# Optimization experiments

Hardware: AMD Instinct MI355X
Metric: run time of the kernel (lower is better)

## Reference

```python
import jax, jax.numpy as jnp
import numpy as np

# ProbAttention (Yangskm/DroneMA-i-), eval mode (dropout=identity).
# Key facts from the source: mask_flag=False, scale=None -> `if self.scale` is
# False, so scores are NOT divided by sqrt(D). The _prob_QK sampling/topk result
# `u` and _get_initial_context are dead code w.r.t. the returned context, so the
# output is exactly dense softmax attention. Inputs are (B, L, H, D); the module
# transposes to (B, H, L, D) and transposes back at the end.

def setup_inputs() -> dict:
    key = jax.random.key(0)
    k1, k2, k3 = jax.random.split(key, 3)
    B, L, H, D = 4, 2048, 8, 64
    return {
        "queries": jax.random.normal(k1, (B, L, H, D), dtype=jnp.float32),
        "keys": jax.random.normal(k2, (B, L, H, D), dtype=jnp.float32),
        "values": jax.random.normal(k3, (B, L, H, D), dtype=jnp.float32),
    }

def reference(queries, keys, values):
    # (B, L, H, D) -> (B, H, L, D)
    q = jnp.swapaxes(queries, 1, 2)
    k = jnp.swapaxes(keys, 1, 2)
    v = jnp.swapaxes(values, 1, 2)
    # dense scores, NO 1/sqrt(D) scaling (scale=None in the original)
    scores = jnp.einsum("bhqd,bhkd->bhqk", q, k)
    attn = jax.nn.softmax(scores, axis=-1)
    ctx = jnp.einsum("bhqk,bhkd->bhqd", attn, v)
    # back to (B, L, H, D)
    return jnp.swapaxes(ctx, 1, 2)
```

## Files before the change

kernel.cpp:

```cpp
#include <hip/hip_runtime.h>
#include <hip/hip_bf16.h>


#define B_ 4
#define L_ 2048
#define H_ 8
#define D_ 64
#define RST_ 512
#define QW_ 32
#define QB_ 128
#define KT_ 64
#define NT_ (L_ / KT_)
#define RS_ 88
#define OTS_ 68
#define SCW_ 35
#define LOG2E_ 1.44269504088896f

#define SMEM_BYTES 45056

typedef _Float16 f16x8 __attribute__((ext_vector_type(8)));
typedef short    s16x4 __attribute__((ext_vector_type(4)));
typedef short    s16x8 __attribute__((ext_vector_type(8)));
typedef float    f32x4 __attribute__((ext_vector_type(4)));

__device__ __forceinline__ unsigned pk_bf16(float a, float b) {
    const __bf16 x = (__bf16)a, y = (__bf16)b;
    return ((unsigned)__builtin_bit_cast(unsigned short, y) << 16) |
           (unsigned)__builtin_bit_cast(unsigned short, x);
}

__device__ __forceinline__ f32x4 mfma16_bf16(s16x4 a, s16x4 b, f32x4 c) {
    return __builtin_amdgcn_mfma_f32_16x16x16bf16_1k(a, b, c, 0, 0, 0);
}

__global__ __launch_bounds__(512, 4) void attn_dbuf_fix(
    const float* __restrict__ Qg, const float* __restrict__ Kg,
    const float* __restrict__ Vg, float* __restrict__ Og)
{
    __shared__ __align__(16) char smem[SMEM_BYTES];
    _Float16* Kf0 = (_Float16*)smem;
    _Float16* Kf1 = (_Float16*)(smem + 11264);
    __bf16*   Vt0 = (__bf16*)(smem + 22528);
    __bf16*   Vt1 = (__bf16*)(smem + 33792);
    float*    Sc  = (float*)smem;

    const int tid  = threadIdx.x;
    const int w    = tid >> 6;
    const int qsub = w & 3;
    const int ks   = w >> 2;
    const int ln   = tid & 15;
    const int lg   = (tid >> 4) & 3;

    const int blk   = (blockIdx.x & 7) * 64 + (blockIdx.x >> 3);
    const int qtile = blk & (L_ / QB_ - 1);
    const int bh    = blk >> 4;
    const int h     = bh & (H_ - 1);
    const int b     = bh >> 3;

    const size_t bhbase = (size_t)b * (L_ * H_ * D_) + (size_t)h * D_;
    const int    qbase  = qtile * QB_ + qsub * QW_;

    f16x8 qf[2][2];
#pragma unroll
    for (int ms = 0; ms < 2; ++ms) {
#pragma unroll
        for (int dc = 0; dc < 2; ++dc) {
            const float* src = Qg + bhbase
                + (size_t)(qbase + ms * 16 + ln) * RST_ + dc * 32 + lg * 8;
            const float4 a = ((const float4*)src)[0];
            const float4 c = ((const float4*)src)[1];
            f16x8 f;
            f[0] = (_Float16)(a.x * LOG2E_); f[1] = (_Float16)(a.y * LOG2E_);
            f[2] = (_Float16)(a.z * LOG2E_); f[3] = (_Float16)(a.w * LOG2E_);
            f[4] = (_Float16)(c.x * LOG2E_); f[5] = (_Float16)(c.y * LOG2E_);
            f[6] = (_Float16)(c.z * LOG2E_); f[7] = (_Float16)(c.w * LOG2E_);
            qf[ms][dc] = f;
        }
    }

    f32x4 o[2][4];
    f32x4 lsum[2];
#pragma unroll
    for (int ms = 0; ms < 2; ++ms) {
        lsum[ms] = (f32x4){0.f, 0.f, 0.f, 0.f};
#pragma unroll
        for (int dg = 0; dg < 4; ++dg) o[ms][dg] = (f32x4){0.f, 0.f, 0.f, 0.f};
    }

    s16x4 ones4;
#pragma unroll
    for (int j = 0; j < 4; ++j) ones4[j] = (short)0x3F80;

    const int krow = tid >> 3;
    const int kd8  = (tid & 7) * 8;
    const int vkp  = (tid & 31) * 2;
    const int vdb  = (tid >> 5) * 4;
    const int vpos = (vkp & 32) + (((vkp & 15) >> 2) * 8)
                   + (((vkp >> 4) & 1) * 4) + (vkp & 3);

    const float* kp = Kg + bhbase + (size_t)krow * RST_ + kd8;
    const float* vp = Vg + bhbase + (size_t)vkp * RST_ + vdb;

    float4 sk0, sk1, sv0, sv1;

    auto issue = [&]() {
        sk0 = ((const float4*)kp)[0];
        sk1 = ((const float4*)kp)[1];
        sv0 = ((const float4*)vp)[0];
        sv1 = ((const float4*)(vp + RST_))[0];
        kp += (size_t)KT_ * RST_;
        vp += (size_t)KT_ * RST_;
    };
    auto writeKV = [&](_Float16* Kf, __bf16* Vt) {
        f16x8 kw;
        kw[0] = (_Float16)sk0.x; kw[1] = (_Float16)sk0.y;
        kw[2] = (_Float16)sk0.z; kw[3] = (_Float16)sk0.w;
        kw[4] = (_Float16)sk1.x; kw[5] = (_Float16)sk1.y;
        kw[6] = (_Float16)sk1.z; kw[7] = (_Float16)sk1.w;
        *(f16x8*)&Kf[krow * RS_ + kd8] = kw;
        *(unsigned*)&Vt[(vdb + 0) * RS_ + vpos] = pk_bf16(sv0.x, sv1.x);
        *(unsigned*)&Vt[(vdb + 1) * RS_ + vpos] = pk_bf16(sv0.y, sv1.y);
        *(unsigned*)&Vt[(vdb + 2) * RS_ + vpos] = pk_bf16(sv0.z, sv1.z);
        *(unsigned*)&Vt[(vdb + 3) * RS_ + vpos] = pk_bf16(sv0.w, sv1.w);
    };

    f16x8 kfr[2][2];
    s16x8 vfp[4];
    auto readFrags = [&](const _Float16* Kf, const __bf16* Vt) {
#pragma unroll
        for (int dc = 0; dc < 2; ++dc)
#pragma unroll
            for (int kg = 0; kg < 2; ++kg)
                kfr[dc][kg] = *(const f16x8*)
                    &Kf[(ks * 32 + kg * 16 + ln) * RS_ + dc * 32 + lg * 8];
#pragma unroll
        for (int dg = 0; dg < 4; ++dg)
            vfp[dg] = *(const s16x8*)&Vt[(dg * 16 + ln) * RS_ + ks * 32 + lg * 8];
    };

    auto computeT = [&]() {
#pragma unroll
        for (int ms = 0; ms < 2; ++ms) {
            f32x4 st[2];
#pragma unroll
            for (int kg = 0; kg < 2; ++kg) st[kg] = (f32x4){0.f, 0.f, 0.f, 0.f};
            __builtin_amdgcn_s_setprio(1);
#pragma unroll
            for (int dc = 0; dc < 2; ++dc)
#pragma unroll
                for (int kg = 0; kg < 2; ++kg)
                    st[kg] = __builtin_amdgcn_mfma_f32_16x16x32_f16(
                        kfr[dc][kg], qf[ms][dc], st[kg], 0, 0, 0);
            __builtin_amdgcn_s_setprio(0);

            s16x4 pf[2];
#pragma unroll
            for (int kg = 0; kg < 2; ++kg) {
                const float p0 = __builtin_amdgcn_exp2f(st[kg][0]);
                const float p1 = __builtin_amdgcn_exp2f(st[kg][1]);
                const float p2 = __builtin_amdgcn_exp2f(st[kg][2]);
                const float p3 = __builtin_amdgcn_exp2f(st[kg][3]);
                union { unsigned u[2]; s16x4 v; } pu;
                pu.u[0] = pk_bf16(p0, p1);
                pu.u[1] = pk_bf16(p2, p3);
                pf[kg] = pu.v;
            }

            __builtin_amdgcn_s_setprio(1);
#pragma unroll
            for (int kg = 0; kg < 2; ++kg) {
                lsum[ms] = mfma16_bf16(ones4, pf[kg], lsum[ms]);
#pragma unroll
                for (int dg = 0; dg < 4; ++dg) {
                    const s16x4 vh = (kg == 0)
                        ? __builtin_shufflevector(vfp[dg], vfp[dg], 0, 1, 2, 3)
                        : __builtin_shufflevector(vfp[dg], vfp[dg], 4, 5, 6, 7);
                    o[ms][dg] = mfma16_bf16(vh, pf[kg], o[ms][dg]);
                }
            }
            __builtin_amdgcn_s_setprio(0);
        }
    };

    issue();
    writeKV(Kf0, Vt0);
    issue();
    __syncthreads();

    for (int t = 0; t < NT_; t += 2) {
        readFrags(Kf0, Vt0);
        writeKV(Kf1, Vt1);
        if (t + 2 < NT_) issue();
        computeT();
        __syncthreads();
        readFrags(Kf1, Vt1);
        if (t + 2 < NT_) writeKV(Kf0, Vt0);
        if (t + 3 < NT_) issue();
        computeT();
        __syncthreads();
    }

    const int lane = tid & 63;
    if (w >= 4) {
        float* sc = &Sc[((w - 4) * 64 + lane) * SCW_];
#pragma unroll
        for (int ms = 0; ms < 2; ++ms)
#pragma unroll
            for (int dg = 0; dg < 4; ++dg)
#pragma unroll
                for (int r = 0; r < 4; ++r)
                    sc[ms * 16 + dg * 4 + r] = o[ms][dg][r];
        sc[32] = lsum[0][0];
        sc[33] = lsum[1][0];
    }
    __syncthreads();
    if (w < 4) {
        const float* sc = &Sc[(w * 64 + lane) * SCW_];
        float po[2][4][4];
#pragma unroll
        for (int ms = 0; ms < 2; ++ms)
#pragma unroll
            for (int dg = 0; dg < 4; ++dg)
#pragma unroll
                for (int r = 0; r < 4; ++r)
                    po[ms][dg][r] = o[ms][dg][r] + sc[ms * 16 + dg * 4 + r];
        const float linv[2] = {1.0f / (lsum[0][0] + sc[32]),
                               1.0f / (lsum[1][0] + sc[33])};

        float* Ot = (float*)(smem + w * 8960);
        const int qr = lane >> 2;
        const int ch = lane & 3;
#pragma unroll
        for (int ms = 0; ms < 2; ++ms) {
#pragma unroll
            for (int dg = 0; dg < 4; ++dg) {
#pragma unroll
                for (int i = 0; i < 2; ++i) {
                    float2 pr;
                    pr.x = po[ms][dg][2 * i]     * linv[ms];
                    pr.y = po[ms][dg][2 * i + 1] * linv[ms];
                    *(float2*)&Ot[ln * OTS_ + dg * 16 + lg * 4 + 2 * i] = pr;
                }
            }
#pragma unroll
            for (int p = 0; p < 4; ++p) {
                const float4 vo = *(const float4*)&Ot[qr * OTS_ + ch * 4 + p * 16];
                *(float4*)(Og + bhbase
                    + (size_t)(qbase + ms * 16 + qr) * RST_ + ch * 4 + p * 16) = vo;
            }
        }
    }
}

extern "C" void kernel_launch(void* const* d_in, const int* in_sizes, int n_in,
                              void* d_out, int out_size, void* d_ws, size_t ws_size,
                              hipStream_t stream) {
    const float* Q = (const float*)d_in[0];
    const float* K = (const float*)d_in[1];
    const float* V = (const float*)d_in[2];
    float* O = (float*)d_out;

    const int grid = B_ * H_ * (L_ / QB_);
    attn_dbuf_fix<<<grid, 512, 0, stream>>>(Q, K, V, O);
}
```

Before: 63.86 us.

## Double block to 1024 threads with 16 query rows per wave

Doubles the threads per block to 1024 and gives each wave 16 query rows instead of 32. This cuts per-wave registers so more waves can be resident, hiding the latency of the LDS reads and the exp computations. K and V tile loading is now split so half the threads load K and half load V, and the V transpose drops the permuted position layout. Fragments are read from LDS inside the compute step rather than ahead of the writes, and the final reduction across the two K-split halves is adapted to 8 query subgroups. In exchange, each K/V fragment read from LDS now serves only 16 query rows, so LDS read traffic per flop doubles.

```diff
diff --git a/kernel.cpp b/kernel.cpp
--- a/kernel.cpp
+++ b/kernel.cpp
@@ -7,20 +7,19 @@
 #define H_ 8
 #define D_ 64
 #define RST_ 512
-#define QW_ 32
+#define QW_ 16
 #define QB_ 128
 #define KT_ 64
 #define NT_ (L_ / KT_)
 #define RS_ 88
 #define OTS_ 68
-#define SCW_ 35
+#define SCW_ 18
 #define LOG2E_ 1.44269504088896f
 
 #define SMEM_BYTES 45056
 
 typedef _Float16 f16x8 __attribute__((ext_vector_type(8)));
 typedef short    s16x4 __attribute__((ext_vector_type(4)));
-typedef short    s16x8 __attribute__((ext_vector_type(8)));
 typedef float    f32x4 __attribute__((ext_vector_type(4)));
 
 __device__ __forceinline__ unsigned pk_bf16(float a, float b) {
@@ -33,7 +32,7 @@
     return __builtin_amdgcn_mfma_f32_16x16x16bf16_1k(a, b, c, 0, 0, 0);
 }
 
-__global__ __launch_bounds__(512, 4) void attn_dbuf_fix(
+__global__ __launch_bounds__(1024, 8) void attn_occ8(
     const float* __restrict__ Qg, const float* __restrict__ Kg,
     const float* __restrict__ Vg, float* __restrict__ Og)
 {
@@ -46,8 +45,8 @@
 
     const int tid  = threadIdx.x;
     const int w    = tid >> 6;
-    const int qsub = w & 3;
-    const int ks   = w >> 2;
+    const int qsub = w & 7;
+    const int ks   = w >> 3;
     const int ln   = tid & 15;
     const int lg   = (tid >> 4) & 3;
 
@@ -60,124 +59,99 @@
     const size_t bhbase = (size_t)b * (L_ * H_ * D_) + (size_t)h * D_;
     const int    qbase  = qtile * QB_ + qsub * QW_;
 
-    f16x8 qf[2][2];
-#pragma unroll
-    for (int ms = 0; ms < 2; ++ms) {
-#pragma unroll
-        for (int dc = 0; dc < 2; ++dc) {
-            const float* src = Qg + bhbase
-                + (size_t)(qbase + ms * 16 + ln) * RST_ + dc * 32 + lg * 8;
-            const float4 a = ((const float4*)src)[0];
-            const float4 c = ((const float4*)src)[1];
-            f16x8 f;
-            f[0] = (_Float16)(a.x * LOG2E_); f[1] = (_Float16)(a.y * LOG2E_);
-            f[2] = (_Float16)(a.z * LOG2E_); f[3] = (_Float16)(a.w * LOG2E_);
-            f[4] = (_Float16)(c.x * LOG2E_); f[5] = (_Float16)(c.y * LOG2E_);
-            f[6] = (_Float16)(c.z * LOG2E_); f[7] = (_Float16)(c.w * LOG2E_);
-            qf[ms][dc] = f;
-        }
-    }
-
-    f32x4 o[2][4];
-    f32x4 lsum[2];
-#pragma unroll
-    for (int ms = 0; ms < 2; ++ms) {
-        lsum[ms] = (f32x4){0.f, 0.f, 0.f, 0.f};
-#pragma unroll
-        for (int dg = 0; dg < 4; ++dg) o[ms][dg] = (f32x4){0.f, 0.f, 0.f, 0.f};
-    }
+    f16x8 qf[2];
+#pragma unroll
+    for (int dc = 0; dc < 2; ++dc) {
+        const float* src = Qg + bhbase
+            + (size_t)(qbase + ln) * RST_ + dc * 32 + lg * 8;
+        const float4 a = ((const float4*)src)[0];
+        const float4 c = ((const float4*)src)[1];
+        f16x8 f;
+        f[0] = (_Float16)(a.x * LOG2E_); f[1] = (_Float16)(a.y * LOG2E_);
+        f[2] = (_Float16)(a.z * LOG2E_); f[3] = (_Float16)(a.w * LOG2E_);
+        f[4] = (_Float16)(c.x * LOG2E_); f[5] = (_Float16)(c.y * LOG2E_);
+        f[6] = (_Float16)(c.z * LOG2E_); f[7] = (_Float16)(c.w * LOG2E_);
+        qf[dc] = f;
+    }
+
+    f32x4 o[4];
+    f32x4 lsum;
+    lsum = (f32x4){0.f, 0.f, 0.f, 0.f};
+#pragma unroll
+    for (int dg = 0; dg < 4; ++dg) o[dg] = (f32x4){0.f, 0.f, 0.f, 0.f};
 
     s16x4 ones4;
 #pragma unroll
     for (int j = 0; j < 4; ++j) ones4[j] = (short)0x3F80;
 
-    const int krow = tid >> 3;
-    const int kd8  = (tid & 7) * 8;
-    const int vkp  = (tid & 31) * 2;
-    const int vdb  = (tid >> 5) * 4;
-    const int vpos = (vkp & 32) + (((vkp & 15) >> 2) * 8)
-                   + (((vkp >> 4) & 1) * 4) + (vkp & 3);
-
-    const float* kp = Kg + bhbase + (size_t)krow * RST_ + kd8;
-    const float* vp = Vg + bhbase + (size_t)vkp * RST_ + vdb;
-
-    float4 sk0, sk1, sv0, sv1;
+    const bool isK = (tid < 512);
+    const int  kt_ = tid & 511;
+    const int  krow = kt_ >> 3;
+    const int  kd8  = (kt_ & 7) * 8;
+    const int  vkp  = (kt_ & 31) * 2;
+    const int  vdb  = (kt_ >> 5) * 4;
+
+    const float* gp = isK
+        ? (Kg + bhbase + (size_t)krow * RST_ + kd8)
+        : (Vg + bhbase + (size_t)vkp * RST_ + vdb);
+    const int soff = isK ? 4 : RST_;
+
+    float4 s0, s1;
 
     auto issue = [&]() {
-        sk0 = ((const float4*)kp)[0];
-        sk1 = ((const float4*)kp)[1];
-        sv0 = ((const float4*)vp)[0];
-        sv1 = ((const float4*)(vp + RST_))[0];
-        kp += (size_t)KT_ * RST_;
-        vp += (size_t)KT_ * RST_;
+        s0 = ((const float4*)gp)[0];
+        s1 = *(const float4*)(gp + soff);
+        gp += (size_t)KT_ * RST_;
     };
     auto writeKV = [&](_Float16* Kf, __bf16* Vt) {
-        f16x8 kw;
-        kw[0] = (_Float16)sk0.x; kw[1] = (_Float16)sk0.y;
-        kw[2] = (_Float16)sk0.z; kw[3] = (_Float16)sk0.w;
-        kw[4] = (_Float16)sk1.x; kw[5] = (_Float16)sk1.y;
-        kw[6] = (_Float16)sk1.z; kw[7] = (_Float16)sk1.w;
-        *(f16x8*)&Kf[krow * RS_ + kd8] = kw;
-        *(unsigned*)&Vt[(vdb + 0) * RS_ + vpos] = pk_bf16(sv0.x, sv1.x);
-        *(unsigned*)&Vt[(vdb + 1) * RS_ + vpos] = pk_bf16(sv0.y, sv1.y);
-        *(unsigned*)&Vt[(vdb + 2) * RS_ + vpos] = pk_bf16(sv0.z, sv1.z);
-        *(unsigned*)&Vt[(vdb + 3) * RS_ + vpos] = pk_bf16(sv0.w, sv1.w);
+        if (isK) {
+            f16x8 kw;
+            kw[0] = (_Float16)s0.x; kw[1] = (_Float16)s0.y;
+            kw[2] = (_Float16)s0.z; kw[3] = (_Float16)s0.w;
+            kw[4] = (_Float16)s1.x; kw[5] = (_Float16)s1.y;
+            kw[6] = (_Float16)s1.z; kw[7] = (_Float16)s1.w;
+            *(f16x8*)&Kf[krow * RS_ + kd8] = kw;
+        } else {
+            *(unsigned*)&Vt[(vdb + 0) * RS_ + vkp] = pk_bf16(s0.x, s1.x);
+            *(unsigned*)&Vt[(vdb + 1) * RS_ + vkp] = pk_bf16(s0.y, s1.y);
+            *(unsigned*)&Vt[(vdb + 2) * RS_ + vkp] = pk_bf16(s0.z, s1.z);
+            *(unsigned*)&Vt[(vdb + 3) * RS_ + vkp] = pk_bf16(s0.w, s1.w);
+        }
     };
 
-    f16x8 kfr[2][2];
-    s16x8 vfp[4];
-    auto readFrags = [&](const _Float16* Kf, const __bf16* Vt) {
-#pragma unroll
-        for (int dc = 0; dc < 2; ++dc)
-#pragma unroll
-            for (int kg = 0; kg < 2; ++kg)
-                kfr[dc][kg] = *(const f16x8*)
-                    &Kf[(ks * 32 + kg * 16 + ln) * RS_ + dc * 32 + lg * 8];
-#pragma unroll
-        for (int dg = 0; dg < 4; ++dg)
-            vfp[dg] = *(const s16x8*)&Vt[(dg * 16 + ln) * RS_ + ks * 32 + lg * 8];
-    };
-
-    auto computeT = [&]() {
-#pragma unroll
-        for (int ms = 0; ms < 2; ++ms) {
-            f32x4 st[2];
-#pragma unroll
-            for (int kg = 0; kg < 2; ++kg) st[kg] = (f32x4){0.f, 0.f, 0.f, 0.f};
+    auto computeT = [&](const _Float16* Kf, const __bf16* Vt) {
+#pragma unroll
+        for (int kg = 0; kg < 2; ++kg) {
+            const int krow0 = (ks * 32 + kg * 16 + ln) * RS_;
+            const f16x8 ka = *(const f16x8*)&Kf[krow0 + lg * 8];
+            const f16x8 kb = *(const f16x8*)&Kf[krow0 + 32 + lg * 8];
+            const int vcol = ks * 32 + kg * 16 + lg * 4;
+            const s16x4 v0 = *(const s16x4*)&Vt[(0 * 16 + ln) * RS_ + vcol];
+            const s16x4 v1 = *(const s16x4*)&Vt[(1 * 16 + ln) * RS_ + vcol];
+            const s16x4 v2 = *(const s16x4*)&Vt[(2 * 16 + ln) * RS_ + vcol];
+            const s16x4 v3 = *(const s16x4*)&Vt[(3 * 16 + ln) * RS_ + vcol];
+
+            f32x4 st = (f32x4){0.f, 0.f, 0.f, 0.f};
             __builtin_amdgcn_s_setprio(1);
-#pragma unroll
-            for (int dc = 0; dc < 2; ++dc)
-#pragma unroll
-                for (int kg = 0; kg < 2; ++kg)
-                    st[kg] = __builtin_amdgcn_mfma_f32_16x16x32_f16(
-                        kfr[dc][kg], qf[ms][dc], st[kg], 0, 0, 0);
+            st = __builtin_amdgcn_mfma_f32_16x16x32_f16(ka, qf[0], st, 0, 0, 0);
+            st = __builtin_amdgcn_mfma_f32_16x16x32_f16(kb, qf[1], st, 0, 0, 0);
             __builtin_amdgcn_s_setprio(0);
 
-            s16x4 pf[2];
-#pragma unroll
-            for (int kg = 0; kg < 2; ++kg) {
-                const float p0 = __builtin_amdgcn_exp2f(st[kg][0]);
-                const float p1 = __builtin_amdgcn_exp2f(st[kg][1]);
-                const float p2 = __builtin_amdgcn_exp2f(st[kg][2]);
-                const float p3 = __builtin_amdgcn_exp2f(st[kg][3]);
-                union { unsigned u[2]; s16x4 v; } pu;
-                pu.u[0] = pk_bf16(p0, p1);
-                pu.u[1] = pk_bf16(p2, p3);
-                pf[kg] = pu.v;
-            }
+            const float e0 = __builtin_amdgcn_exp2f(st[0]);
+            const float e1 = __builtin_amdgcn_exp2f(st[1]);
+            const float e2 = __builtin_amdgcn_exp2f(st[2]);
+            const float e3 = __builtin_amdgcn_exp2f(st[3]);
+            union { unsigned u[2]; s16x4 v; } pu;
+            pu.u[0] = pk_bf16(e0, e1);
+            pu.u[1] = pk_bf16(e2, e3);
+            const s16x4 pf = pu.v;
 
             __builtin_amdgcn_s_setprio(1);
-#pragma unroll
-            for (int kg = 0; kg < 2; ++kg) {
-                lsum[ms] = mfma16_bf16(ones4, pf[kg], lsum[ms]);
-#pragma unroll
-                for (int dg = 0; dg < 4; ++dg) {
-                    const s16x4 vh = (kg == 0)
-                        ? __builtin_shufflevector(vfp[dg], vfp[dg], 0, 1, 2, 3)
-                        : __builtin_shufflevector(vfp[dg], vfp[dg], 4, 5, 6, 7);
-                    o[ms][dg] = mfma16_bf16(vh, pf[kg], o[ms][dg]);
-                }
-            }
+            lsum = mfma16_bf16(ones4, pf, lsum);
+            o[0] = mfma16_bf16(v0, pf, o[0]);
+            o[1] = mfma16_bf16(v1, pf, o[1]);
+            o[2] = mfma16_bf16(v2, pf, o[2]);
+            o[3] = mfma16_bf16(v3, pf, o[3]);
             __builtin_amdgcn_s_setprio(0);
         }
     };
@@ -188,66 +162,55 @@
     __syncthreads();
 
     for (int t = 0; t < NT_; t += 2) {
-        readFrags(Kf0, Vt0);
+        computeT(Kf0, Vt0);
         writeKV(Kf1, Vt1);
         if (t + 2 < NT_) issue();
-        computeT();
         __syncthreads();
-        readFrags(Kf1, Vt1);
+        computeT(Kf1, Vt1);
         if (t + 2 < NT_) writeKV(Kf0, Vt0);
         if (t + 3 < NT_) issue();
-        computeT();
         __syncthreads();
     }
 
     const int lane = tid & 63;
-    if (w >= 4) {
-        float* sc = &Sc[((w - 4) * 64 + lane) * SCW_];
-#pragma unroll
-        for (int ms = 0; ms < 2; ++ms)
-#pragma unroll
-            for (int dg = 0; dg < 4; ++dg)
-#pragma unroll
-                for (int r = 0; r < 4; ++r)
-                    sc[ms * 16 + dg * 4 + r] = o[ms][dg][r];
-        sc[32] = lsum[0][0];
-        sc[33] = lsum[1][0];
+    if (ks == 1) {
+        float* sc = &Sc[(qsub * 64 + lane) * SCW_];
+#pragma unroll
+        for (int dg = 0; dg < 4; ++dg)
+#pragma unroll
+            for (int r = 0; r < 4; ++r)
+                sc[dg * 4 + r] = o[dg][r];
+        sc[16] = lsum[0];
     }
     __syncthreads();
-    if (w < 4) {
-        const float* sc = &Sc[(w * 64 + lane) * SCW_];
-        float po[2][4][4];
-#pragma unroll
-        for (int ms = 0; ms < 2; ++ms)
-#pragma unroll
-            for (int dg = 0; dg < 4; ++dg)
-#pragma unroll
-                for (int r = 0; r < 4; ++r)
-                    po[ms][dg][r] = o[ms][dg][r] + sc[ms * 16 + dg * 4 + r];
-        const float linv[2] = {1.0f / (lsum[0][0] + sc[32]),
-                               1.0f / (lsum[1][0] + sc[33])};
-
-        float* Ot = (float*)(smem + w * 8960);
+    if (ks == 0) {
+        const float* sc = &Sc[(qsub * 64 + lane) * SCW_];
+        float po[4][4];
+#pragma unroll
+        for (int dg = 0; dg < 4; ++dg)
+#pragma unroll
+            for (int r = 0; r < 4; ++r)
+                po[dg][r] = o[dg][r] + sc[dg * 4 + r];
+        const float linv = 1.0f / (lsum[0] + sc[16]);
+
+        float* Ot = (float*)(smem + qsub * (64 * SCW_ * 4));
         const int qr = lane >> 2;
         const int ch = lane & 3;
 #pragma unroll
-        for (int ms = 0; ms < 2; ++ms) {
-#pragma unroll
-            for (int dg = 0; dg < 4; ++dg) {
-#pragma unroll
-                for (int i = 0; i < 2; ++i) {
-                    float2 pr;
-                    pr.x = po[ms][dg][2 * i]     * linv[ms];
-                    pr.y = po[ms][dg][2 * i + 1] * linv[ms];
-                    *(float2*)&Ot[ln * OTS_ + dg * 16 + lg * 4 + 2 * i] = pr;
-                }
+        for (int dg = 0; dg < 4; ++dg) {
+#pragma unroll
+            for (int i = 0; i < 2; ++i) {
+                float2 pr;
+                pr.x = po[dg][2 * i]     * linv;
+                pr.y = po[dg][2 * i + 1] * linv;
+                *(float2*)&Ot[ln * OTS_ + dg * 16 + lg * 4 + 2 * i] = pr;
             }
-#pragma unroll
-            for (int p = 0; p < 4; ++p) {
-                const float4 vo = *(const float4*)&Ot[qr * OTS_ + ch * 4 + p * 16];
-                *(float4*)(Og + bhbase
-                    + (size_t)(qbase + ms * 16 + qr) * RST_ + ch * 4 + p * 16) = vo;
-            }
+        }
+#pragma unroll
+        for (int p = 0; p < 4; ++p) {
+            const float4 vo = *(const float4*)&Ot[qr * OTS_ + ch * 4 + p * 16];
+            *(float4*)(Og + bhbase
+                + (size_t)(qbase + qr) * RST_ + ch * 4 + p * 16) = vo;
         }
     }
 }
@@ -261,5 +224,5 @@
     float* O = (float*)d_out;
 
     const int grid = B_ * H_ * (L_ / QB_);
-    attn_dbuf_fix<<<grid, 512, 0, stream>>>(Q, K, V, O);
-}
+    attn_occ8<<<grid, 1024, 0, stream>>>(Q, K, V, O);
+}
```

New measurement: 95.22 us. +49.1%, slower.
